# Kernel optimization log

Measured on AMD Instinct MI355X. Metric: run time of the kernel, lower is better.

Reference implementation:

```python
import jax, jax.numpy as jnp
import numpy as np

E = 512        # emb_size
H = 2 * E      # LSTM units
B = 512        # beam/query batch (batched Python-loop states)
K = 32         # padded candidates per state
T = 8          # max_path_length
N_ENT = 50000
N_REL = 5000


def setup_inputs() -> dict:
    key = jax.random.key(0)
    ks = jax.random.split(key, 12)
    f32 = jnp.float32
    ent_emb = jax.random.normal(ks[0], (N_ENT, E), f32) * 0.05
    rel_emb = jax.random.normal(ks[1], (N_REL, E), f32) * 0.05
    relation = jax.random.normal(ks[2], (B, E), f32) * 0.05
    Wx = jax.random.normal(ks[3], (H, 4 * H), f32) * 0.02
    Wh = jax.random.normal(ks[4], (H, 4 * H), f32) * 0.02
    b = jnp.zeros((4 * H,), f32)
    W1 = jax.random.normal(ks[5], (4 * E, 3 * E), f32) * 0.02
    b1 = jnp.zeros((3 * E,), f32)
    W2 = jax.random.normal(ks[6], (3 * E, 2 * E), f32) * 0.02
    b2 = jnp.zeros((2 * E,), f32)
    current_ids = jax.random.randint(ks[7], (T, B), 0, N_ENT)
    prev_rel_ids = jax.random.randint(ks[8], (T, B), 0, N_REL)
    cand_rel_ids = jax.random.randint(ks[9], (T, B, K), 0, N_REL)
    cand_ent_ids = jax.random.randint(ks[10], (T, B, K), 0, N_ENT)
    return {
        "ent_emb": ent_emb, "rel_emb": rel_emb, "relation": relation,
        "Wx": Wx, "Wh": Wh, "b": b,
        "W1": W1, "b1": b1, "W2": W2, "b2": b2,
        "current_ids": current_ids, "prev_rel_ids": prev_rel_ids,
        "cand_rel_ids": cand_rel_ids, "cand_ent_ids": cand_ent_ids,
    }


def reference(ent_emb, rel_emb, relation, Wx, Wh, b, W1, b1, W2, b2,
              current_ids, prev_rel_ids, cand_rel_ids, cand_ent_ids):
    Bh = relation.shape[0]
    units = Wh.shape[0]
    h0 = jnp.zeros((Bh, units), ent_emb.dtype)
    c0 = jnp.zeros((Bh, units), ent_emb.dtype)

    def step(carry, xs):
        h, c = carry
        cur, prl, crel, cent = xs
        # LSTMCell input: concat(prev relation vec, current entity vec)  [B, 2E]
        x = jnp.concatenate([rel_emb[prl], ent_emb[cur]], axis=-1)
        z = x @ Wx + h @ Wh + b                      # [B, 4H], keras gate order i,f,g,o
        i_, f_, g_, o_ = jnp.split(z, 4, axis=-1)
        c = jax.nn.sigmoid(f_) * c + jax.nn.sigmoid(i_) * jnp.tanh(g_)
        h = jax.nn.sigmoid(o_) * jnp.tanh(c)
        # posterior MLP on concat(ent, history, relation)  [B, 4E] -> [B, 2E]
        feat = jax.nn.relu(jnp.concatenate([ent_emb[cur], h, relation], axis=-1) @ W1 + b1)
        feat = jax.nn.relu(feat @ W2 + b2)
        # candidate embeddings: concat(rel vec, to-entity vec)  [B, K, 2E]
        cand = jnp.concatenate([rel_emb[crel], ent_emb[cent]], axis=-1)
        probs = jax.nn.softmax(jnp.einsum('bkd,bd->bk', cand, feat), axis=-1)
        return (h, c), probs

    _, probs = jax.lax.scan(step, (h0, c0),
                            (current_ids, prev_rel_ids, cand_rel_ids, cand_ent_ids))
    return probs  # [T, B, K]
```

## Files before the change

kernel.cpp:

```cpp
#include <hip/hip_runtime.h>
#include <stdint.h>

typedef __attribute__((ext_vector_type(4))) float f32x4;
typedef __attribute__((ext_vector_type(8))) __bf16 bf16x8;
typedef __attribute__((ext_vector_type(8))) unsigned short u16x8;
typedef __attribute__((ext_vector_type(4))) unsigned short u16x4;

typedef const __attribute__((address_space(1))) unsigned int gu32;
typedef __attribute__((address_space(3))) unsigned int lu32;

__device__ __forceinline__ float b2f(unsigned short u) {
  unsigned int x = ((unsigned int)u) << 16;
  float f; __builtin_memcpy(&f, &x, 4); return f;
}
__device__ __forceinline__ unsigned short f2b(float f) {
  unsigned int x; __builtin_memcpy(&x, &f, 4);
  x += 0x7fffu + ((x >> 16) & 1u);
  return (unsigned short)(x >> 16);
}
__device__ __forceinline__ float sigmoidf(float x) {
  return 1.f / (1.f + __expf(-x));
}
__device__ __forceinline__ float tanh_fast(float x) {
  return 1.f - 2.f / (1.f + __expf(2.f * x));
}

__global__ __launch_bounds__(256) void conv_all(
    const float* __restrict__ ent, unsigned short* __restrict__ entB,
    const float* __restrict__ rel, unsigned short* __restrict__ relB,
    const float* __restrict__ rln, unsigned short* __restrict__ rlnB) {
  const long long N0 = 50000LL * 512 / 8, N1 = 5000LL * 512 / 8, N2 = 512LL * 512 / 8;
  long long i = (long long)blockIdx.x * 256 + threadIdx.x;
  if (i >= N0 + N1 + N2) return;
  const float* in; unsigned short* out;
  if (i < N0)            { in = ent; out = entB; }
  else if (i < N0 + N1)  { in = rel; out = relB; i -= N0; }
  else                   { in = rln; out = rlnB; i -= N0 + N1; }
  f32x4 a = *(const f32x4*)(in + i * 8);
  f32x4 b = *(const f32x4*)(in + i * 8 + 4);
  unsigned short t[8];
#pragma unroll
  for (int j = 0; j < 4; j++) { t[j] = f2b(a[j]); t[4+j] = f2b(b[j]); }
  *(u16x8*)(out + i * 8) = *(u16x8*)t;
}

__global__ __launch_bounds__(256) void transpose_all(
    const float* __restrict__ Wx, unsigned short* __restrict__ WxT,
    const float* __restrict__ Wh, unsigned short* __restrict__ WhT,
    const float* __restrict__ W1, unsigned short* __restrict__ W1T,
    const float* __restrict__ W2, unsigned short* __restrict__ W2T) {
  __shared__ unsigned short tile[64][72];
  int b = blockIdx.x;
  const float* in; unsigned short* out; int R, C, bx, by;
  if (b < 1024)      { in = Wx; out = WxT; R = 1024; C = 4096; bx = b & 63; by = b >> 6; }
  else if (b < 2048) { b -= 1024; in = Wh; out = WhT; R = 1024; C = 4096; bx = b & 63; by = b >> 6; }
  else if (b < 2816) { b -= 2048; in = W1; out = W1T; R = 2048; C = 1536; bx = b % 24; by = b / 24; }
  else               { b -= 2816; in = W2; out = W2T; R = 1536; C = 1024; bx = b & 15; by = b >> 4; }
  const int r0 = by * 64, c0 = bx * 64;
  const int tid = threadIdx.x;
  const int r = tid >> 3;
  const int c8 = (tid & 7) * 8;
#pragma unroll
  for (int i = 0; i < 2; i++) {
    const float* src = in + (size_t)(r0 + r + 32*i) * C + c0 + c8;
    f32x4 a = *(const f32x4*)src;
    f32x4 bb = *(const f32x4*)(src + 4);
    unsigned short tmp[8];
#pragma unroll
    for (int j = 0; j < 4; j++) { tmp[j] = f2b(a[j]); tmp[4+j] = f2b(bb[j]); }
    *(u16x8*)(&tile[r + 32*i][c8]) = *(u16x8*)tmp;
  }
  __syncthreads();
#pragma unroll
  for (int i = 0; i < 2; i++) {
    const int ro = r + 32*i;
    unsigned short tmp[8];
#pragma unroll
    for (int j = 0; j < 8; j++) tmp[j] = tile[c8 + j][ro];
    *(u16x8*)(out + (size_t)(c0 + ro) * R + r0 + c8) = *(u16x8*)tmp;
  }
}

__global__ void gather_all(const unsigned short* __restrict__ entB,
                           const unsigned short* __restrict__ relB,
                           const unsigned short* __restrict__ relationB,
                           const int* __restrict__ cur, const int* __restrict__ prl,
                           unsigned short* __restrict__ Xall,
                           unsigned short* __restrict__ ERall) {
  const int row = blockIdx.x;
  const int b = row & 511;
  const int tid = threadIdx.x;
  const int ci = cur[row], ri = prl[row];
  const unsigned short* xsrc = (tid < 64) ? (relB + (size_t)ri * 512 + tid * 8)
                                          : (entB + (size_t)ci * 512 + (tid - 64) * 8);
  const unsigned short* esrc = (tid < 64) ? (entB + (size_t)ci * 512 + tid * 8)
                                          : (relationB + (size_t)b * 512 + (tid - 64) * 8);
  *(u16x8*)(Xall + (size_t)row * 1024 + tid * 8) = *(const u16x8*)xsrc;
  *(u16x8*)(ERall + (size_t)row * 1024 + tid * 8) = *(const u16x8*)esrc;
}

template<bool HAS_BIAS, bool DO_RELU, bool PERM_B, bool ASPLIT, bool GLD>
__global__ __launch_bounds__(256) void gemm_bf16(
    const unsigned short* __restrict__ A,
    const unsigned short* __restrict__ A2, int lda,
    const unsigned short* __restrict__ BT, int ldb, int K,
    const float* __restrict__ bias,
    unsigned short* __restrict__ Cout, int ldc) {
  constexpr int LDP = GLD ? 64 : 72;
  __shared__ unsigned short As[128][LDP];
  __shared__ unsigned short Bs[128][LDP];
  const int tid = threadIdx.x;
  const int lane = tid & 63;
  const int w = tid >> 6;
  const int wr = w >> 1, wc = w & 1;
  const int m0 = blockIdx.y * 128, n0 = blockIdx.x * 128;
  f32x4 acc[4][4] = {};
  const int rs = tid >> 3;
  const int cs = (tid & 7) * 8;
  const int srow = lane >> 3;
  const int scol = (lane & 7) * 8;

  for (int k0 = 0; k0 < K; k0 += 64) {
    const unsigned short* asrc; int ac;
    if (ASPLIT) {
      if (k0 < 512)       { asrc = A;  ac = k0; }
      else if (k0 < 1536) { asrc = A2; ac = k0 - 512; }
      else                { asrc = A;  ac = k0 - 1024; }
    } else { asrc = A; ac = k0; }
    if (GLD) {
#pragma unroll
      for (int i = 0; i < 4; i++) {
        const int c = w * 4 + i;
        const int row = c * 8 + srow;
        __builtin_amdgcn_global_load_lds(
            (gu32*)(asrc + (size_t)(m0 + row) * lda + ac + scol),
            (lu32*)(&As[0][0] + c * 512), 16, 0, 0);
        const int brow = n0 + row;
        const int prow = PERM_B ? (((brow & 3) << 10) + (brow >> 2)) : brow;
        __builtin_amdgcn_global_load_lds(
            (gu32*)(BT + (size_t)prow * ldb + k0 + scol),
            (lu32*)(&Bs[0][0] + c * 512), 16, 0, 0);
      }
    } else {
#pragma unroll
      for (int i = 0; i < 4; i++)
        *(u16x8*)(&As[rs + 32*i][cs]) =
            *(const u16x8*)(asrc + (size_t)(m0 + rs + 32*i) * lda + ac + cs);
#pragma unroll
      for (int i = 0; i < 4; i++) {
        const int brow = n0 + rs + 32*i;
        const int prow = PERM_B ? (((brow & 3) << 10) + (brow >> 2)) : brow;
        *(u16x8*)(&Bs[rs + 32*i][cs]) =
            *(const u16x8*)(BT + (size_t)prow * ldb + k0 + cs);
      }
    }
    __syncthreads();
#pragma unroll
    for (int ks = 0; ks < 2; ks++) {
      const int kb = ks * 32 + (lane >> 4) * 8;
      bf16x8 af[4], bfr[4];
#pragma unroll
      for (int m = 0; m < 4; m++)
        af[m] = *reinterpret_cast<const bf16x8*>(&As[wr*64 + m*16 + (lane & 15)][kb]);
#pragma unroll
      for (int n = 0; n < 4; n++)
        bfr[n] = *reinterpret_cast<const bf16x8*>(&Bs[wc*64 + n*16 + (lane & 15)][kb]);
#pragma unroll
      for (int m = 0; m < 4; m++)
#pragma unroll
        for (int n = 0; n < 4; n++)
          acc[m][n] = __builtin_amdgcn_mfma_f32_16x16x32_bf16(af[m], bfr[n], acc[m][n], 0, 0, 0);
    }
    __syncthreads();
  }

  const int cn = lane & 15, rb = (lane >> 4) * 4;
#pragma unroll
  for (int m = 0; m < 4; m++) {
#pragma unroll
    for (int n = 0; n < 4; n++) {
      const int gn = n0 + wc*64 + n*16 + cn;
#pragma unroll
      for (int r = 0; r < 4; r++) {
        const int gm = m0 + wr*64 + m*16 + rb + r;
        float v = acc[m][n][r];
        if (HAS_BIAS) v += bias[gn];
        if (DO_RELU)  v = v > 0.f ? v : 0.f;
        Cout[(size_t)gm * ldc + gn] = f2b(v);
      }
    }
  }
}

__global__ __launch_bounds__(512) void zgemm_lstm(
    const unsigned short* __restrict__ A,
    const unsigned short* __restrict__ BT,
    const unsigned short* __restrict__ pre,
    const float* __restrict__ bias,
    unsigned short* __restrict__ Hout,
    float* __restrict__ Cst) {
  __shared__ unsigned short As[2][64][72];
  __shared__ unsigned short Bs[2][128][72];
  __shared__ f32x4 accL[8][256];
  const int tid = threadIdx.x;
  const int lane = tid & 63;
  const int w = tid >> 6;
  const int q = w >> 2;
  const int wq = w & 3;
  const int wr = wq >> 1, wc = wq & 1;
  const int m0 = blockIdx.y * 64, n0 = blockIdx.x * 128;
  f32x4 acc[2][4] = {};
  const int tq = tid & 255;
  const int rs = tq >> 3;
  const int cs = (tq & 7) * 8;

  for (int k0 = 0; k0 < 512; k0 += 64) {
    const int kk = q * 512 + k0;
#pragma unroll
    for (int i = 0; i < 2; i++)
      *(u16x8*)(&As[q][rs + 32*i][cs]) =
          *(const u16x8*)(A + (size_t)(m0 + rs + 32*i) * 1024 + kk + cs);
#pragma unroll
    for (int i = 0; i < 4; i++) {
      const int brow = n0 + rs + 32*i;
      const int prow = ((brow & 3) << 10) + (brow >> 2);
      *(u16x8*)(&Bs[q][rs + 32*i][cs]) =
          *(const u16x8*)(BT + (size_t)prow * 1024 + kk + cs);
    }
    __syncthreads();
#pragma unroll
    for (int ks = 0; ks < 2; ks++) {
      const int kb = ks * 32 + (lane >> 4) * 8;
      bf16x8 af[2], bfr[4];
#pragma unroll
      for (int m = 0; m < 2; m++)
        af[m] = *reinterpret_cast<const bf16x8*>(&As[q][wr*32 + m*16 + (lane & 15)][kb]);
#pragma unroll
      for (int n = 0; n < 4; n++)
        bfr[n] = *reinterpret_cast<const bf16x8*>(&Bs[q][wc*64 + n*16 + (lane & 15)][kb]);
#pragma unroll
      for (int m = 0; m < 2; m++)
#pragma unroll
        for (int n = 0; n < 4; n++)
          acc[m][n] = __builtin_amdgcn_mfma_f32_16x16x32_bf16(af[m], bfr[n], acc[m][n], 0, 0, 0);
    }
    __syncthreads();
  }

  if (q == 1) {
#pragma unroll
    for (int m = 0; m < 2; m++)
#pragma unroll
      for (int n = 0; n < 4; n++)
        accL[m*4 + n][tq] = acc[m][n];
  }
  __syncthreads();
  if (q == 0) {
    const int cn = lane & 15, rb = (lane >> 4) * 4, g = lane & 3;
#pragma unroll
    for (int m = 0; m < 2; m++) {
#pragma unroll
      for (int n = 0; n < 4; n++) {
        const f32x4 s4 = accL[m*4 + n][tq];
        const int gn = n0 + wc*64 + n*16 + cn;
        const int u = gn >> 2;
        const float gb = bias[g * 1024 + u];
        const int row0 = m0 + wr*32 + m*16 + rb;
        const float v0 = acc[m][n][0] + s4[0] + b2f(pre[(size_t)(row0+0) * 4096 + gn]) + gb;
        const float v1 = acc[m][n][1] + s4[1] + b2f(pre[(size_t)(row0+1) * 4096 + gn]) + gb;
        const float v2 = acc[m][n][2] + s4[2] + b2f(pre[(size_t)(row0+2) * 4096 + gn]) + gb;
        const float v3 = acc[m][n][3] + s4[3] + b2f(pre[(size_t)(row0+3) * 4096 + gn]) + gb;
        auto sel = [&](int idx) {
          return idx == 0 ? v0 : idx == 1 ? v1 : idx == 2 ? v2 : v3;
        };
        const float own = sel(g);
        const float r1 = __shfl_xor(sel(g ^ 1), 1);
        const float r2 = __shfl_xor(sel(g ^ 2), 2);
        const float r3 = __shfl_xor(sel(g ^ 3), 3);
        const float zi = g==0 ? own : g==1 ? r1 : g==2 ? r2 : r3;
        const float zf = g==0 ? r1  : g==1 ? own: g==2 ? r3 : r2;
        const float zg_= g==0 ? r2  : g==1 ? r3 : g==2 ? own: r1;
        const float zo = g==0 ? r3  : g==1 ? r2 : g==2 ? r1 : own;
        const size_t hidx = (size_t)(row0 + g) * 1024 + u;
        const float cnew = sigmoidf(zf) * Cst[hidx] + sigmoidf(zi) * tanh_fast(zg_);
        const float h = sigmoidf(zo) * tanh_fast(cnew);
        Cst[hidx] = cnew;
        Hout[hidx] = f2b(h);
      }
    }
  }
}

__global__ void lstm_gate0(const unsigned short* __restrict__ P1_,
                           const float* __restrict__ bias,
                           float* __restrict__ C, unsigned short* __restrict__ H) {
  const int idx = blockIdx.x * 256 + threadIdx.x;
  const int b = idx >> 10, u = idx & 1023;
  u16x4 z4 = *(const u16x4*)(P1_ + (size_t)b * 4096 + 4 * u);
  const float i_ = b2f(z4[0]) + bias[u];
  const float g_ = b2f(z4[2]) + bias[2048 + u];
  const float o_ = b2f(z4[3]) + bias[3072 + u];
  const float c = sigmoidf(i_) * tanh_fast(g_);
  const float h = sigmoidf(o_) * tanh_fast(c);
  C[idx] = c;
  H[idx] = f2b(h);
}

__global__ __launch_bounds__(256) void score_softmax(
    const unsigned short* __restrict__ F2,
    const unsigned short* __restrict__ relB,
    const unsigned short* __restrict__ entB,
    const int* __restrict__ crel, const int* __restrict__ cent,
    float* __restrict__ outp) {
  const int b = blockIdx.x;
  const int tid = threadIdx.x;
  const int lane = tid & 63, w = tid >> 6;
  __shared__ float feat[1024];
  __shared__ float logits[32];
  {
    u16x4 fv = ((const u16x4*)(F2 + (size_t)b * 1024))[tid];
#pragma unroll
    for (int j = 0; j < 4; j++) feat[tid * 4 + j] = b2f(fv[j]);
  }
  __syncthreads();
  for (int k = w; k < 32; k += 4) {
    const int ri = crel[b * 32 + k], ei = cent[b * 32 + k];
    u16x8 rv = *(const u16x8*)(relB + (size_t)ri * 512 + lane * 8);
    u16x8 ev = *(const u16x8*)(entB + (size_t)ei * 512 + lane * 8);
    float sum = 0.f;
#pragma unroll
    for (int j = 0; j < 8; j++) {
      sum += b2f(rv[j]) * feat[lane * 8 + j];
      sum += b2f(ev[j]) * feat[512 + lane * 8 + j];
    }
#pragma unroll
    for (int off = 32; off; off >>= 1) sum += __shfl_down(sum, off, 64);
    if (lane == 0) logits[k] = sum;
  }
  __syncthreads();
  if (tid < 32) {
    const float l = logits[tid];
    float mx = l;
#pragma unroll
    for (int off = 16; off; off >>= 1) mx = fmaxf(mx, __shfl_xor(mx, off, 32));
    const float p = __expf(l - mx);
    float s = p;
#pragma unroll
    for (int off = 16; off; off >>= 1) s += __shfl_xor(s, off, 32);
    outp[(size_t)b * 32 + tid] = p / s;
  }
}

extern "C" void kernel_launch(void* const* d_in, const int* in_sizes, int n_in,
                              void* d_out, int out_size, void* d_ws, size_t ws_size,
                              hipStream_t stream) {
  const float* ent      = (const float*)d_in[0];
  const float* rel      = (const float*)d_in[1];
  const float* relation = (const float*)d_in[2];
  const float* Wx       = (const float*)d_in[3];
  const float* Wh       = (const float*)d_in[4];
  const float* bvec     = (const float*)d_in[5];
  const float* W1       = (const float*)d_in[6];
  const float* b1       = (const float*)d_in[7];
  const float* W2       = (const float*)d_in[8];
  const float* b2       = (const float*)d_in[9];
  const int* cur  = (const int*)d_in[10];
  const int* prl  = (const int*)d_in[11];
  const int* crel = (const int*)d_in[12];
  const int* cent = (const int*)d_in[13];
  float* out = (float*)d_out;
  (void)in_sizes; (void)n_in; (void)out_size; (void)ws_size;

  char* wsp = (char*)d_ws;
  auto alloc = [&](size_t bytes) { char* p = wsp; wsp += (bytes + 255) & ~(size_t)255; return p; };
  unsigned short* entB = (unsigned short*)alloc((size_t)50000 * 512 * 2);
  unsigned short* relB = (unsigned short*)alloc((size_t)5000 * 512 * 2);
  unsigned short* rlnB = (unsigned short*)alloc((size_t)512 * 512 * 2);
  unsigned short* WxT  = (unsigned short*)alloc((size_t)4096 * 1024 * 2);
  unsigned short* WhT  = (unsigned short*)alloc((size_t)4096 * 1024 * 2);
  unsigned short* W1T  = (unsigned short*)alloc((size_t)1536 * 2048 * 2);
  unsigned short* W2T  = (unsigned short*)alloc((size_t)1024 * 1536 * 2);
  unsigned short* Xall = (unsigned short*)alloc((size_t)4096 * 1024 * 2);
  unsigned short* ERall= (unsigned short*)alloc((size_t)4096 * 1024 * 2);
  unsigned short* P1   = (unsigned short*)alloc((size_t)4096 * 4096 * 2);
  unsigned short* Hall = (unsigned short*)alloc((size_t)4096 * 1024 * 2);
  unsigned short* F1   = (unsigned short*)alloc((size_t)4096 * 1536 * 2);
  unsigned short* F2   = (unsigned short*)alloc((size_t)4096 * 1024 * 2);
  float*          C    = (float*)         alloc((size_t)512 * 1024 * 4);

  const dim3 blk(256);
  const size_t HS = (size_t)512 * 1024;

  {
    const long long tot = 50000LL*512/8 + 5000LL*512/8 + 512LL*512/8;
    conv_all<<<(unsigned)((tot + 255) / 256), blk, 0, stream>>>(
        ent, entB, rel, relB, relation, rlnB);
  }
  transpose_all<<<3200, blk, 0, stream>>>(Wx, WxT, Wh, WhT, W1, W1T, W2, W2T);
  gather_all<<<4096, 128, 0, stream>>>(entB, relB, rlnB, cur, prl, Xall, ERall);

  gemm_bf16<false,false,true,false,true><<<dim3(32, 32), blk, 0, stream>>>(
      Xall, nullptr, 1024, WxT, 1024, 1024, nullptr, P1, 4096);

  lstm_gate0<<<2048, 256, 0, stream>>>(P1, bvec, C, Hall);
  for (int t = 1; t < 8; t++) {
    zgemm_lstm<<<dim3(32, 8), dim3(512), 0, stream>>>(
        Hall + (size_t)(t - 1) * HS, WhT,
        P1 + (size_t)t * 512 * 4096, bvec,
        Hall + (size_t)t * HS, C);
  }

  gemm_bf16<true,true,false,true,true><<<dim3(12, 32), blk, 0, stream>>>(
      ERall, Hall, 1024, W1T, 2048, 2048, b1, F1, 1536);
  gemm_bf16<true,true,false,false,true><<<dim3(8, 32), blk, 0, stream>>>(
      F1, nullptr, 1536, W2T, 1536, 1536, b2, F2, 1024);
  score_softmax<<<4096, 256, 0, stream>>>(F2, relB, entB, crel, cent, out);
}
```

Measured before the change: 353.3 us.

## Fuse LSTM timestep loop into one cooperative persistent kernel with register cell state

Replaces the gate0 kernel and the seven per-step recurrent GEMM launches with a single cooperative kernel. It loops over timesteps with grid-wide syncs and keeps the cell state in registers instead of global memory, which removes launch gaps and C-state traffic. It also drops the direct global-to-LDS load path from the generic GEMM and uses only register-staged loads. That second change may cost some speed in the large GEMMs, and the cooperative launch depends on all 256 blocks being co-resident.

```diff
diff --git a/kernel.cpp b/kernel.cpp
--- a/kernel.cpp
+++ b/kernel.cpp
@@ -1,13 +1,13 @@
 #include <hip/hip_runtime.h>
+#include <hip/hip_cooperative_groups.h>
 #include <stdint.h>
+
+namespace cg = cooperative_groups;
 
 typedef __attribute__((ext_vector_type(4))) float f32x4;
 typedef __attribute__((ext_vector_type(8))) __bf16 bf16x8;
 typedef __attribute__((ext_vector_type(8))) unsigned short u16x8;
 typedef __attribute__((ext_vector_type(4))) unsigned short u16x4;
-
-typedef const __attribute__((address_space(1))) unsigned int gu32;
-typedef __attribute__((address_space(3))) unsigned int lu32;
 
 __device__ __forceinline__ float b2f(unsigned short u) {
   unsigned int x = ((unsigned int)u) << 16;
@@ -99,16 +99,15 @@
   *(u16x8*)(ERall + (size_t)row * 1024 + tid * 8) = *(const u16x8*)esrc;
 }
 
-template<bool HAS_BIAS, bool DO_RELU, bool PERM_B, bool ASPLIT, bool GLD>
+template<bool HAS_BIAS, bool DO_RELU, bool PERM_B, bool ASPLIT>
 __global__ __launch_bounds__(256) void gemm_bf16(
     const unsigned short* __restrict__ A,
     const unsigned short* __restrict__ A2, int lda,
     const unsigned short* __restrict__ BT, int ldb, int K,
     const float* __restrict__ bias,
     unsigned short* __restrict__ Cout, int ldc) {
-  constexpr int LDP = GLD ? 64 : 72;
-  __shared__ unsigned short As[128][LDP];
-  __shared__ unsigned short Bs[128][LDP];
+  __shared__ unsigned short As[128][72];
+  __shared__ unsigned short Bs[128][72];
   const int tid = threadIdx.x;
   const int lane = tid & 63;
   const int w = tid >> 6;
@@ -117,8 +116,6 @@
   f32x4 acc[4][4] = {};
   const int rs = tid >> 3;
   const int cs = (tid & 7) * 8;
-  const int srow = lane >> 3;
-  const int scol = (lane & 7) * 8;
 
   for (int k0 = 0; k0 < K; k0 += 64) {
     const unsigned short* asrc; int ac;
@@ -127,32 +124,16 @@
       else if (k0 < 1536) { asrc = A2; ac = k0 - 512; }
       else                { asrc = A;  ac = k0 - 1024; }
     } else { asrc = A; ac = k0; }
-    if (GLD) {
-#pragma unroll
-      for (int i = 0; i < 4; i++) {
-        const int c = w * 4 + i;
-        const int row = c * 8 + srow;
-        __builtin_amdgcn_global_load_lds(
-            (gu32*)(asrc + (size_t)(m0 + row) * lda + ac + scol),
-            (lu32*)(&As[0][0] + c * 512), 16, 0, 0);
-        const int brow = n0 + row;
-        const int prow = PERM_B ? (((brow & 3) << 10) + (brow >> 2)) : brow;
-        __builtin_amdgcn_global_load_lds(
-            (gu32*)(BT + (size_t)prow * ldb + k0 + scol),
-            (lu32*)(&Bs[0][0] + c * 512), 16, 0, 0);
-      }
-    } else {
-#pragma unroll
-      for (int i = 0; i < 4; i++)
-        *(u16x8*)(&As[rs + 32*i][cs]) =
-            *(const u16x8*)(asrc + (size_t)(m0 + rs + 32*i) * lda + ac + cs);
-#pragma unroll
-      for (int i = 0; i < 4; i++) {
-        const int brow = n0 + rs + 32*i;
-        const int prow = PERM_B ? (((brow & 3) << 10) + (brow >> 2)) : brow;
-        *(u16x8*)(&Bs[rs + 32*i][cs]) =
-            *(const u16x8*)(BT + (size_t)prow * ldb + k0 + cs);
-      }
+#pragma unroll
+    for (int i = 0; i < 4; i++)
+      *(u16x8*)(&As[rs + 32*i][cs]) =
+          *(const u16x8*)(asrc + (size_t)(m0 + rs + 32*i) * lda + ac + cs);
+#pragma unroll
+    for (int i = 0; i < 4; i++) {
+      const int brow = n0 + rs + 32*i;
+      const int prow = PERM_B ? (((brow & 3) << 10) + (brow >> 2)) : brow;
+      *(u16x8*)(&Bs[rs + 32*i][cs]) =
+          *(const u16x8*)(BT + (size_t)prow * ldb + k0 + cs);
     }
     __syncthreads();
 #pragma unroll
@@ -192,13 +173,12 @@
   }
 }
 
-__global__ __launch_bounds__(512) void zgemm_lstm(
-    const unsigned short* __restrict__ A,
+__global__ __launch_bounds__(512) void lstm_chain(
+    const unsigned short* __restrict__ P1,
     const unsigned short* __restrict__ BT,
-    const unsigned short* __restrict__ pre,
     const float* __restrict__ bias,
-    unsigned short* __restrict__ Hout,
-    float* __restrict__ Cst) {
+    unsigned short* __restrict__ Hall) {
+  cg::grid_group gg = cg::this_grid();
   __shared__ unsigned short As[2][64][72];
   __shared__ unsigned short Bs[2][128][72];
   __shared__ f32x4 accL[8][256];
@@ -209,101 +189,118 @@
   const int wq = w & 3;
   const int wr = wq >> 1, wc = wq & 1;
   const int m0 = blockIdx.y * 64, n0 = blockIdx.x * 128;
-  f32x4 acc[2][4] = {};
   const int tq = tid & 255;
   const int rs = tq >> 3;
   const int cs = (tq & 7) * 8;
-
-  for (int k0 = 0; k0 < 512; k0 += 64) {
-    const int kk = q * 512 + k0;
-#pragma unroll
-    for (int i = 0; i < 2; i++)
-      *(u16x8*)(&As[q][rs + 32*i][cs]) =
-          *(const u16x8*)(A + (size_t)(m0 + rs + 32*i) * 1024 + kk + cs);
-#pragma unroll
-    for (int i = 0; i < 4; i++) {
-      const int brow = n0 + rs + 32*i;
-      const int prow = ((brow & 3) << 10) + (brow >> 2);
-      *(u16x8*)(&Bs[q][rs + 32*i][cs]) =
-          *(const u16x8*)(BT + (size_t)prow * 1024 + kk + cs);
+  const int cn = lane & 15, rb = (lane >> 4) * 4, g = lane & 3;
+  const size_t HS = (size_t)512 * 1024;
+
+  float C_reg[2][4];
+  int urow[2], ucol[4]; float gb4[4][4];
+  float gbias[4];
+#pragma unroll
+  for (int m = 0; m < 2; m++) urow[m] = m0 + wr*32 + m*16 + rb;
+#pragma unroll
+  for (int n = 0; n < 4; n++) ucol[n] = (n0 + wc*64 + n*16 + cn) >> 2;
+
+  if (q == 0) {
+#pragma unroll
+    for (int m = 0; m < 2; m++) {
+#pragma unroll
+      for (int n = 0; n < 4; n++) {
+        const int row = urow[m] + g, u = ucol[n];
+        u16x4 z4 = *(const u16x4*)(P1 + (size_t)row * 4096 + 4 * u);
+        const float i_ = b2f(z4[0]) + bias[u];
+        const float g_ = b2f(z4[2]) + bias[2048 + u];
+        const float o_ = b2f(z4[3]) + bias[3072 + u];
+        const float c = sigmoidf(i_) * tanh_fast(g_);
+        const float h = sigmoidf(o_) * tanh_fast(c);
+        C_reg[m][n] = c;
+        Hall[(size_t)row * 1024 + u] = f2b(h);
+      }
+    }
+  }
+  gg.sync();
+
+  for (int t = 1; t < 8; t++) {
+    const unsigned short* A = Hall + (size_t)(t - 1) * HS;
+    const unsigned short* pre = P1 + (size_t)t * 512 * 4096;
+    f32x4 acc[2][4] = {};
+    for (int k0 = 0; k0 < 512; k0 += 64) {
+      const int kk = q * 512 + k0;
+#pragma unroll
+      for (int i = 0; i < 2; i++)
+        *(u16x8*)(&As[q][rs + 32*i][cs]) =
+            *(const u16x8*)(A + (size_t)(m0 + rs + 32*i) * 1024 + kk + cs);
+#pragma unroll
+      for (int i = 0; i < 4; i++) {
+        const int brow = n0 + rs + 32*i;
+        const int prow = ((brow & 3) << 10) + (brow >> 2);
+        *(u16x8*)(&Bs[q][rs + 32*i][cs]) =
+            *(const u16x8*)(BT + (size_t)prow * 1024 + kk + cs);
+      }
+      __syncthreads();
+#pragma unroll
+      for (int ks = 0; ks < 2; ks++) {
+        const int kb = ks * 32 + (lane >> 4) * 8;
+        bf16x8 af[2], bfr[4];
+#pragma unroll
+        for (int m = 0; m < 2; m++)
+          af[m] = *reinterpret_cast<const bf16x8*>(&As[q][wr*32 + m*16 + (lane & 15)][kb]);
+#pragma unroll
+        for (int n = 0; n < 4; n++)
+          bfr[n] = *reinterpret_cast<const bf16x8*>(&Bs[q][wc*64 + n*16 + (lane & 15)][kb]);
+#pragma unroll
+        for (int m = 0; m < 2; m++)
+#pragma unroll
+          for (int n = 0; n < 4; n++)
+            acc[m][n] = __builtin_amdgcn_mfma_f32_16x16x32_bf16(af[m], bfr[n], acc[m][n], 0, 0, 0);
+      }
+      __syncthreads();
+    }
+
+    if (q == 1) {
+#pragma unroll
+      for (int m = 0; m < 2; m++)
+#pragma unroll
+        for (int n = 0; n < 4; n++)
+          accL[m*4 + n][tq] = acc[m][n];
     }
     __syncthreads();
-#pragma unroll
-    for (int ks = 0; ks < 2; ks++) {
-      const int kb = ks * 32 + (lane >> 4) * 8;
-      bf16x8 af[2], bfr[4];
-#pragma unroll
-      for (int m = 0; m < 2; m++)
-        af[m] = *reinterpret_cast<const bf16x8*>(&As[q][wr*32 + m*16 + (lane & 15)][kb]);
-#pragma unroll
-      for (int n = 0; n < 4; n++)
-        bfr[n] = *reinterpret_cast<const bf16x8*>(&Bs[q][wc*64 + n*16 + (lane & 15)][kb]);
-#pragma unroll
-      for (int m = 0; m < 2; m++)
-#pragma unroll
-        for (int n = 0; n < 4; n++)
-          acc[m][n] = __builtin_amdgcn_mfma_f32_16x16x32_bf16(af[m], bfr[n], acc[m][n], 0, 0, 0);
-    }
-    __syncthreads();
-  }
-
-  if (q == 1) {
-#pragma unroll
-    for (int m = 0; m < 2; m++)
-#pragma unroll
-      for (int n = 0; n < 4; n++)
-        accL[m*4 + n][tq] = acc[m][n];
-  }
-  __syncthreads();
-  if (q == 0) {
-    const int cn = lane & 15, rb = (lane >> 4) * 4, g = lane & 3;
-#pragma unroll
-    for (int m = 0; m < 2; m++) {
-#pragma unroll
-      for (int n = 0; n < 4; n++) {
-        const f32x4 s4 = accL[m*4 + n][tq];
-        const int gn = n0 + wc*64 + n*16 + cn;
-        const int u = gn >> 2;
-        const float gb = bias[g * 1024 + u];
-        const int row0 = m0 + wr*32 + m*16 + rb;
-        const float v0 = acc[m][n][0] + s4[0] + b2f(pre[(size_t)(row0+0) * 4096 + gn]) + gb;
-        const float v1 = acc[m][n][1] + s4[1] + b2f(pre[(size_t)(row0+1) * 4096 + gn]) + gb;
-        const float v2 = acc[m][n][2] + s4[2] + b2f(pre[(size_t)(row0+2) * 4096 + gn]) + gb;
-        const float v3 = acc[m][n][3] + s4[3] + b2f(pre[(size_t)(row0+3) * 4096 + gn]) + gb;
-        auto sel = [&](int idx) {
-          return idx == 0 ? v0 : idx == 1 ? v1 : idx == 2 ? v2 : v3;
-        };
-        const float own = sel(g);
-        const float r1 = __shfl_xor(sel(g ^ 1), 1);
-        const float r2 = __shfl_xor(sel(g ^ 2), 2);
-        const float r3 = __shfl_xor(sel(g ^ 3), 3);
-        const float zi = g==0 ? own : g==1 ? r1 : g==2 ? r2 : r3;
-        const float zf = g==0 ? r1  : g==1 ? own: g==2 ? r3 : r2;
-        const float zg_= g==0 ? r2  : g==1 ? r3 : g==2 ? own: r1;
-        const float zo = g==0 ? r3  : g==1 ? r2 : g==2 ? r1 : own;
-        const size_t hidx = (size_t)(row0 + g) * 1024 + u;
-        const float cnew = sigmoidf(zf) * Cst[hidx] + sigmoidf(zi) * tanh_fast(zg_);
-        const float h = sigmoidf(zo) * tanh_fast(cnew);
-        Cst[hidx] = cnew;
-        Hout[hidx] = f2b(h);
+    if (q == 0) {
+#pragma unroll
+      for (int m = 0; m < 2; m++) {
+#pragma unroll
+        for (int n = 0; n < 4; n++) {
+          const f32x4 s4 = accL[m*4 + n][tq];
+          const int gn = n0 + wc*64 + n*16 + cn;
+          const int u = ucol[n];
+          const float gb = bias[g * 1024 + u];
+          const int row0 = urow[m];
+          const float v0 = acc[m][n][0] + s4[0] + b2f(pre[(size_t)(row0+0) * 4096 + gn]) + gb;
+          const float v1 = acc[m][n][1] + s4[1] + b2f(pre[(size_t)(row0+1) * 4096 + gn]) + gb;
+          const float v2 = acc[m][n][2] + s4[2] + b2f(pre[(size_t)(row0+2) * 4096 + gn]) + gb;
+          const float v3 = acc[m][n][3] + s4[3] + b2f(pre[(size_t)(row0+3) * 4096 + gn]) + gb;
+          auto sel = [&](int idx) {
+            return idx == 0 ? v0 : idx == 1 ? v1 : idx == 2 ? v2 : v3;
+          };
+          const float own = sel(g);
+          const float r1 = __shfl_xor(sel(g ^ 1), 1);
+          const float r2 = __shfl_xor(sel(g ^ 2), 2);
+          const float r3 = __shfl_xor(sel(g ^ 3), 3);
+          const float zi = g==0 ? own : g==1 ? r1 : g==2 ? r2 : r3;
+          const float zf = g==0 ? r1  : g==1 ? own: g==2 ? r3 : r2;
+          const float zg_= g==0 ? r2  : g==1 ? r3 : g==2 ? own: r1;
+          const float zo = g==0 ? r3  : g==1 ? r2 : g==2 ? r1 : own;
+          const float cnew = sigmoidf(zf) * C_reg[m][n] + sigmoidf(zi) * tanh_fast(zg_);
+          const float h = sigmoidf(zo) * tanh_fast(cnew);
+          C_reg[m][n] = cnew;
+          Hall[(size_t)t * HS + (size_t)(row0 + g) * 1024 + u] = f2b(h);
+        }
       }
     }
-  }
-}
-
-__global__ void lstm_gate0(const unsigned short* __restrict__ P1_,
-                           const float* __restrict__ bias,
-                           float* __restrict__ C, unsigned short* __restrict__ H) {
-  const int idx = blockIdx.x * 256 + threadIdx.x;
-  const int b = idx >> 10, u = idx & 1023;
-  u16x4 z4 = *(const u16x4*)(P1_ + (size_t)b * 4096 + 4 * u);
-  const float i_ = b2f(z4[0]) + bias[u];
-  const float g_ = b2f(z4[2]) + bias[2048 + u];
-  const float o_ = b2f(z4[3]) + bias[3072 + u];
-  const float c = sigmoidf(i_) * tanh_fast(g_);
-  const float h = sigmoidf(o_) * tanh_fast(c);
-  C[idx] = c;
-  H[idx] = f2b(h);
+    gg.sync();
+  }
 }
 
 __global__ __launch_bounds__(256) void score_softmax(
@@ -386,10 +383,8 @@
   unsigned short* Hall = (unsigned short*)alloc((size_t)4096 * 1024 * 2);
   unsigned short* F1   = (unsigned short*)alloc((size_t)4096 * 1536 * 2);
   unsigned short* F2   = (unsigned short*)alloc((size_t)4096 * 1024 * 2);
-  float*          C    = (float*)         alloc((size_t)512 * 1024 * 4);
 
   const dim3 blk(256);
-  const size_t HS = (size_t)512 * 1024;
 
   {
     const long long tot = 50000LL*512/8 + 5000LL*512/8 + 512LL*512/8;
@@ -399,20 +394,22 @@
   transpose_all<<<3200, blk, 0, stream>>>(Wx, WxT, Wh, WhT, W1, W1T, W2, W2T);
   gather_all<<<4096, 128, 0, stream>>>(entB, relB, rlnB, cur, prl, Xall, ERall);
 
-  gemm_bf16<false,false,true,false,true><<<dim3(32, 32), blk, 0, stream>>>(
+  gemm_bf16<false,false,true,false><<<dim3(32, 32), blk, 0, stream>>>(
       Xall, nullptr, 1024, WxT, 1024, 1024, nullptr, P1, 4096);
 
-  lstm_gate0<<<2048, 256, 0, stream>>>(P1, bvec, C, Hall);
-  for (int t = 1; t < 8; t++) {
-    zgemm_lstm<<<dim3(32, 8), dim3(512), 0, stream>>>(
-        Hall + (size_t)(t - 1) * HS, WhT,
-        P1 + (size_t)t * 512 * 4096, bvec,
-        Hall + (size_t)t * HS, C);
-  }
-
-  gemm_bf16<true,true,false,true,true><<<dim3(12, 32), blk, 0, stream>>>(
+  {
+    const unsigned short* P1a = P1;
+    const unsigned short* BTa = WhT;
+    const float* ba = bvec;
+    unsigned short* Ha = Hall;
+    void* kargs[] = { (void*)&P1a, (void*)&BTa, (void*)&ba, (void*)&Ha };
+    hipLaunchCooperativeKernel((void*)lstm_chain, dim3(32, 8), dim3(512),
+                               kargs, 0, stream);
+  }
+
+  gemm_bf16<true,true,false,true><<<dim3(12, 32), blk, 0, stream>>>(
       ERall, Hall, 1024, W1T, 2048, 2048, b1, F1, 1536);
-  gemm_bf16<true,true,false,false,true><<<dim3(8, 32), blk, 0, stream>>>(
+  gemm_bf16<true,true,false,false><<<dim3(8, 32), blk, 0, stream>>>(
       F1, nullptr, 1536, W2T, 1536, 1536, b2, F2, 1024);
   score_softmax<<<4096, 256, 0, stream>>>(F2, relB, entB, crel, cent, out);
 }
```

After: 572.1 us. +61.9%, slower.

## Fuse step-0 LSTM gate into input GEMM epilogue, drop direct-to-LDS loads

Applied to the files above, without the earlier changes.

Removes the separate lstm_gate0 kernel. For the first 512 rows, the input-projection GEMM now computes the t=0 LSTM cell and hidden state in its epilogue, using lane shuffles to gather the four interleaved gates. Those blocks skip writing P1 rows for step 0. It also replaces the global_load_lds path with register-staged loads into padded LDS tiles for all GEMMs. That removes the async direct-to-LDS copies, which may cost some load throughput.

```diff
diff --git a/kernel.cpp b/kernel.cpp
--- a/kernel.cpp
+++ b/kernel.cpp
@@ -5,9 +5,6 @@
 typedef __attribute__((ext_vector_type(8))) __bf16 bf16x8;
 typedef __attribute__((ext_vector_type(8))) unsigned short u16x8;
 typedef __attribute__((ext_vector_type(4))) unsigned short u16x4;
-
-typedef const __attribute__((address_space(1))) unsigned int gu32;
-typedef __attribute__((address_space(3))) unsigned int lu32;
 
 __device__ __forceinline__ float b2f(unsigned short u) {
   unsigned int x = ((unsigned int)u) << 16;
@@ -99,16 +96,17 @@
   *(u16x8*)(ERall + (size_t)row * 1024 + tid * 8) = *(const u16x8*)esrc;
 }
 
-template<bool HAS_BIAS, bool DO_RELU, bool PERM_B, bool ASPLIT, bool GLD>
+template<bool HAS_BIAS, bool DO_RELU, bool PERM_B, bool ASPLIT, bool LSTM0>
 __global__ __launch_bounds__(256) void gemm_bf16(
     const unsigned short* __restrict__ A,
     const unsigned short* __restrict__ A2, int lda,
     const unsigned short* __restrict__ BT, int ldb, int K,
     const float* __restrict__ bias,
-    unsigned short* __restrict__ Cout, int ldc) {
-  constexpr int LDP = GLD ? 64 : 72;
-  __shared__ unsigned short As[128][LDP];
-  __shared__ unsigned short Bs[128][LDP];
+    unsigned short* __restrict__ Cout, int ldc,
+    const float* __restrict__ gbias,
+    unsigned short* __restrict__ Hout, float* __restrict__ Cst) {
+  __shared__ unsigned short As[128][72];
+  __shared__ unsigned short Bs[128][72];
   const int tid = threadIdx.x;
   const int lane = tid & 63;
   const int w = tid >> 6;
@@ -117,8 +115,6 @@
   f32x4 acc[4][4] = {};
   const int rs = tid >> 3;
   const int cs = (tid & 7) * 8;
-  const int srow = lane >> 3;
-  const int scol = (lane & 7) * 8;
 
   for (int k0 = 0; k0 < K; k0 += 64) {
     const unsigned short* asrc; int ac;
@@ -127,32 +123,16 @@
       else if (k0 < 1536) { asrc = A2; ac = k0 - 512; }
       else                { asrc = A;  ac = k0 - 1024; }
     } else { asrc = A; ac = k0; }
-    if (GLD) {
-#pragma unroll
-      for (int i = 0; i < 4; i++) {
-        const int c = w * 4 + i;
-        const int row = c * 8 + srow;
-        __builtin_amdgcn_global_load_lds(
-            (gu32*)(asrc + (size_t)(m0 + row) * lda + ac + scol),
-            (lu32*)(&As[0][0] + c * 512), 16, 0, 0);
-        const int brow = n0 + row;
-        const int prow = PERM_B ? (((brow & 3) << 10) + (brow >> 2)) : brow;
-        __builtin_amdgcn_global_load_lds(
-            (gu32*)(BT + (size_t)prow * ldb + k0 + scol),
-            (lu32*)(&Bs[0][0] + c * 512), 16, 0, 0);
-      }
-    } else {
-#pragma unroll
-      for (int i = 0; i < 4; i++)
-        *(u16x8*)(&As[rs + 32*i][cs]) =
-            *(const u16x8*)(asrc + (size_t)(m0 + rs + 32*i) * lda + ac + cs);
-#pragma unroll
-      for (int i = 0; i < 4; i++) {
-        const int brow = n0 + rs + 32*i;
-        const int prow = PERM_B ? (((brow & 3) << 10) + (brow >> 2)) : brow;
-        *(u16x8*)(&Bs[rs + 32*i][cs]) =
-            *(const u16x8*)(BT + (size_t)prow * ldb + k0 + cs);
-      }
+#pragma unroll
+    for (int i = 0; i < 4; i++)
+      *(u16x8*)(&As[rs + 32*i][cs]) =
+          *(const u16x8*)(asrc + (size_t)(m0 + rs + 32*i) * lda + ac + cs);
+#pragma unroll
+    for (int i = 0; i < 4; i++) {
+      const int brow = n0 + rs + 32*i;
+      const int prow = PERM_B ? (((brow & 3) << 10) + (brow >> 2)) : brow;
+      *(u16x8*)(&Bs[rs + 32*i][cs]) =
+          *(const u16x8*)(BT + (size_t)prow * ldb + k0 + cs);
     }
     __syncthreads();
 #pragma unroll
@@ -175,6 +155,39 @@
   }
 
   const int cn = lane & 15, rb = (lane >> 4) * 4;
+  if (LSTM0 && m0 < 512) {
+    const int g = lane & 3;
+#pragma unroll
+    for (int m = 0; m < 4; m++) {
+#pragma unroll
+      for (int n = 0; n < 4; n++) {
+        const int gn = n0 + wc*64 + n*16 + cn;
+        const int u = gn >> 2;
+        const float gb = gbias[g * 1024 + u];
+        const int row0 = m0 + wr*64 + m*16 + rb;
+        const float v0 = acc[m][n][0] + gb;
+        const float v1 = acc[m][n][1] + gb;
+        const float v2 = acc[m][n][2] + gb;
+        const float v3 = acc[m][n][3] + gb;
+        auto sel = [&](int idx) {
+          return idx == 0 ? v0 : idx == 1 ? v1 : idx == 2 ? v2 : v3;
+        };
+        const float own = sel(g);
+        const float r1 = __shfl_xor(sel(g ^ 1), 1);
+        const float r2 = __shfl_xor(sel(g ^ 2), 2);
+        const float r3 = __shfl_xor(sel(g ^ 3), 3);
+        const float zi = g==0 ? own : g==1 ? r1 : g==2 ? r2 : r3;
+        const float zg_= g==0 ? r2  : g==1 ? r3 : g==2 ? own: r1;
+        const float zo = g==0 ? r3  : g==1 ? r2 : g==2 ? r1 : own;
+        const float cnew = sigmoidf(zi) * tanh_fast(zg_);
+        const float h = sigmoidf(zo) * tanh_fast(cnew);
+        const size_t hidx = (size_t)(row0 + g) * 1024 + u;
+        Cst[hidx] = cnew;
+        Hout[hidx] = f2b(h);
+      }
+    }
+    return;
+  }
 #pragma unroll
   for (int m = 0; m < 4; m++) {
 #pragma unroll
@@ -291,21 +304,6 @@
   }
 }
 
-__global__ void lstm_gate0(const unsigned short* __restrict__ P1_,
-                           const float* __restrict__ bias,
-                           float* __restrict__ C, unsigned short* __restrict__ H) {
-  const int idx = blockIdx.x * 256 + threadIdx.x;
-  const int b = idx >> 10, u = idx & 1023;
-  u16x4 z4 = *(const u16x4*)(P1_ + (size_t)b * 4096 + 4 * u);
-  const float i_ = b2f(z4[0]) + bias[u];
-  const float g_ = b2f(z4[2]) + bias[2048 + u];
-  const float o_ = b2f(z4[3]) + bias[3072 + u];
-  const float c = sigmoidf(i_) * tanh_fast(g_);
-  const float h = sigmoidf(o_) * tanh_fast(c);
-  C[idx] = c;
-  H[idx] = f2b(h);
-}
-
 __global__ __launch_bounds__(256) void score_softmax(
     const unsigned short* __restrict__ F2,
     const unsigned short* __restrict__ relB,
@@ -400,9 +398,8 @@
   gather_all<<<4096, 128, 0, stream>>>(entB, relB, rlnB, cur, prl, Xall, ERall);
 
   gemm_bf16<false,false,true,false,true><<<dim3(32, 32), blk, 0, stream>>>(
-      Xall, nullptr, 1024, WxT, 1024, 1024, nullptr, P1, 4096);
-
-  lstm_gate0<<<2048, 256, 0, stream>>>(P1, bvec, C, Hall);
+      Xall, nullptr, 1024, WxT, 1024, 1024, nullptr, P1, 4096, bvec, Hall, C);
+
   for (int t = 1; t < 8; t++) {
     zgemm_lstm<<<dim3(32, 8), dim3(512), 0, stream>>>(
         Hall + (size_t)(t - 1) * HS, WhT,
@@ -410,9 +407,9 @@
         Hall + (size_t)t * HS, C);
   }
 
-  gemm_bf16<true,true,false,true,true><<<dim3(12, 32), blk, 0, stream>>>(
-      ERall, Hall, 1024, W1T, 2048, 2048, b1, F1, 1536);
-  gemm_bf16<true,true,false,false,true><<<dim3(8, 32), blk, 0, stream>>>(
-      F1, nullptr, 1536, W2T, 1536, 1536, b2, F2, 1024);
+  gemm_bf16<true,true,false,true,false><<<dim3(12, 32), blk, 0, stream>>>(
+      ERall, Hall, 1024, W1T, 2048, 2048, b1, F1, 1536, nullptr, nullptr, nullptr);
+  gemm_bf16<true,true,false,false,false><<<dim3(8, 32), blk, 0, stream>>>(
+      F1, nullptr, 1536, W2T, 1536, 1536, b2, F2, 1024, nullptr, nullptr, nullptr);
   score_softmax<<<4096, 256, 0, stream>>>(F2, relB, entB, crel, cent, out);
 }
```

Result: faster. 336.5 us (-4.8%).
